# Kernel tuning notes

Hardware: AMD Instinct MI355X
Metric: run time of the kernel (lower is better)

The kernel has to match this reference:

```python
import jax, jax.numpy as jnp
import numpy as np

B, C, NMAX = 256, 1, 256   # graphs, channels, max nodes per graph
N = B * C * NMAX           # total nodes = 65536
E = N * 16                 # edges = 1,048,576
EMB, HID = 128, 128


def setup_inputs() -> dict:
    key = jax.random.key(0)
    ks = jax.random.split(key, 8)
    adj = jax.random.uniform(ks[0], (B, C, NMAX, NMAX), jnp.float32)
    edges = jax.random.randint(ks[1], (E, 2), 0, N, dtype=jnp.int32)
    subgraph_idx = jnp.repeat(jnp.arange(B, dtype=jnp.int32), C * NMAX)
    def lin(k, fan_in, fan_out):
        return jax.random.normal(k, (fan_in, fan_out), jnp.float32) / np.sqrt(fan_in).astype(np.float32)
    return {
        "adj": adj, "edges": edges, "subgraph_idx": subgraph_idx,
        "Wdec": lin(ks[2], NMAX, EMB), "bdec": jnp.zeros((EMB,), jnp.float32),
        "Wc1": lin(ks[3], EMB, HID),   "bc1": jnp.zeros((HID,), jnp.float32),
        "Wc2": lin(ks[4], HID, HID),   "bc2": jnp.zeros((HID,), jnp.float32),
        "Wp1": lin(ks[5], HID, HID),   "bp1": jnp.zeros((HID,), jnp.float32),
        "Wp2": lin(ks[6], HID, 1),     "bp2": jnp.zeros((1,), jnp.float32),
    }


def gcn_conv(x, W, b, src, dst):
    # PyG GCNConv: h = x W; add self-loops; symmetric normalization D^-1/2 (A+I) D^-1/2; + bias
    h = x @ W                                      # [N, out]
    deg = jnp.zeros((N,), x.dtype).at[dst].add(1.0) + 1.0  # in-degree incl. self loop
    dinv = jax.lax.rsqrt(deg)                      # [N]
    coef = dinv[src] * dinv[dst]                   # [E]
    agg = jax.ops.segment_sum(h[src] * coef[:, None], dst, num_segments=N)
    return agg + h * (dinv * dinv)[:, None] + b    # self-loop term + bias


def reference(adj, edges, subgraph_idx, Wdec, bdec, Wc1, bc1, Wc2, bc2, Wp1, bp1, Wp2, bp2):
    src, dst = edges[:, 0], edges[:, 1]
    # decoder_input: Linear(max_num_nodes -> embedding_dim) on flattened adjacency rows
    x = adj.reshape(-1, NMAX) @ Wdec + bdec        # [N, EMB]
    # forward applies convs[:-1] only (2 of the 3 convs); dropout is identity in eval mode
    x = jax.nn.relu(gcn_conv(x, Wc1, bc1, src, dst))
    x = jax.nn.relu(gcn_conv(x, Wc2, bc2, src, dst))
    # global max pool over nodes of each graph
    pooled = jax.ops.segment_max(x, subgraph_idx, num_segments=B)  # [B, HID]
    # post_mp MLP head
    h = jax.nn.relu(pooled @ Wp1 + bp1)
    return h @ Wp2 + bp2                           # [B, 1]
```

## Files before the change

kernel.cpp:

```cpp
#include <hip/hip_runtime.h>
#include <hip/hip_fp16.h>
#include <cstdint>
#include <cstddef>

#define NN   65536
#define NE   1048576
#define FD   128
#define KDEC 256
#define NGRAPH 256
#define NEP_MAX (NE + 15 * NN)
#define DUMMY_SRC 65536u
#define EPB  4096
#define BCAP 4608

typedef __attribute__((ext_vector_type(8))) short s16x8;
typedef __attribute__((ext_vector_type(4))) float f32x4;

__device__ __forceinline__ ushort f2bf(float x) {
  uint u = __float_as_uint(x);
  uint r = (u + 0x7fffu + ((u >> 16) & 1u)) >> 16;
  return (ushort)r;
}
__device__ __forceinline__ float bf2f(ushort h) {
  return __uint_as_float(((uint)h) << 16);
}


__global__ __launch_bounds__(1024) void k_histbin(const int* __restrict__ edges,
                                                  uint* __restrict__ binbuf,
                                                  int* __restrict__ gbin) {
  const int b = blockIdx.x, t = threadIdx.x;
  __shared__ int lcnt[256];
  __shared__ int lsum[256];
  __shared__ int gbase[256];
  __shared__ uint sorted[EPB];

  if (t < 256) lcnt[t] = 0;
  __syncthreads();

  uint rec[4];
  ushort bkt[4], lidx[4];
#pragma unroll
  for (int r = 0; r < 4; r++) {
    int i = b * EPB + r * 1024 + t;
    int2 e = ((const int2*)edges)[i];
    int bucket = e.y >> 8;
    int li = atomicAdd(&lcnt[bucket], 1);
    rec[r] = ((uint)bucket << 24) | ((uint)(e.y & 255) << 16) | (uint)e.x;
    bkt[r] = (ushort)bucket;
    lidx[r] = (ushort)li;
  }
  __syncthreads();

  if (t < 256) lsum[t] = lcnt[t];
  __syncthreads();
  for (int off = 1; off < 256; off <<= 1) {
    int v = 0;
    if (t < 256 && t >= off) v = lsum[t - off];
    __syncthreads();
    if (t < 256) lsum[t] += v;
    __syncthreads();
  }
  if (t < 256) gbase[t] = atomicAdd(&gbin[t], lcnt[t]);
  __syncthreads();

#pragma unroll
  for (int r = 0; r < 4; r++) {
    int B = bkt[r];
    sorted[lsum[B] - lcnt[B] + lidx[r]] = rec[r];
  }
  __syncthreads();

  for (int s = t; s < EPB; s += 1024) {
    uint v = sorted[s];
    int B = v >> 24;
    int ex = lsum[B] - lcnt[B];
    binbuf[B * BCAP + gbase[B] + (s - ex)] = v & 0xFFFFFFu;
  }
}

__device__ __forceinline__ void prep_one(const float* __restrict__ W,
                                         ushort* __restrict__ H,
                                         ushort* __restrict__ L, int i) {
  int k = i >> 7, c = i & 127;
  float w = W[i];
  ushort h = f2bf(w);
  ushort lo = f2bf(w - bf2f(h));
  size_t dst = ((size_t)((k >> 5) * 8 + (c >> 4)) * 64 +
                (size_t)((c & 15) + 16 * ((k & 31) >> 3))) * 8 + (k & 7);
  H[dst] = h;
  L[dst] = lo;
}

__global__ __launch_bounds__(256) void k_misc1(const uint* __restrict__ binbuf,
                                               const int* __restrict__ gbin,
                                               int* __restrict__ hist,
                                               int* __restrict__ bsum,
                                               const float* __restrict__ Wdec,
                                               const float* __restrict__ Wc1,
                                               const float* __restrict__ bdec,
                                               float* __restrict__ wfused,
                                               float* __restrict__ bfused,
                                               const float* __restrict__ Wc2,
                                               ushort* __restrict__ w2h,
                                               ushort* __restrict__ w2l) {
  int b = blockIdx.x, t = threadIdx.x;
  if (b < 256) {
    __shared__ int lc[256];
    __shared__ int s[256];
    lc[t] = 0;
    __syncthreads();
    int m = gbin[b];
    for (int i = t; i < m; i += 256)
      atomicAdd(&lc[binbuf[b * BCAP + i] >> 16], 1);
    __syncthreads();
    hist[b * 256 + t] = lc[t];
    s[t] = (lc[t] + 15) & ~15;
    __syncthreads();
    for (int st = 128; st > 0; st >>= 1) {
      if (t < st) s[t] += s[t + st];
      __syncthreads();
    }
    if (t == 0) bsum[b] = s[0];
  } else if (b < 384) {
    int i = (b - 256) * 256 + t;
    int k = i >> 7, c = i & 127;
    float acc = 0.f;
#pragma unroll 8
    for (int j = 0; j < 128; j++) acc = fmaf(Wdec[k * FD + j], Wc1[j * FD + c], acc);
    wfused[i] = acc;
    if (b == 256 && t < 128) {
      float ba = 0.f;
      for (int j = 0; j < 128; j++) ba = fmaf(bdec[j], Wc1[j * FD + t], ba);
      bfused[t] = ba;
    }
  } else {
    int i = (b - 384) * 256 + t;
    prep_one(Wc2, w2h, w2l, i);
  }
}

__global__ __launch_bounds__(256) void k_misc2(const int* __restrict__ hist,
                                               const int* __restrict__ bsum,
                                               int* __restrict__ offs,
                                               float* __restrict__ dinv,
                                               const float* __restrict__ wfused,
                                               ushort* __restrict__ wfh,
                                               ushort* __restrict__ wfl,
                                               const uint* __restrict__ binbuf,
                                               const int* __restrict__ gbin,
                                               uint* __restrict__ ec) {
  int b = blockIdx.x, t = threadIdx.x;
  if (b < 256) {
    __shared__ int sb[256];
    __shared__ int s[256];
    __shared__ int sofs[256];
    __shared__ int cnt2[256];
    sb[t] = bsum[t];
    int v = hist[b * 256 + t];
    int vp = (v + 15) & ~15;
    s[t] = vp;
    __syncthreads();
    for (int off = 1; off < 256; off <<= 1) {
      int addb = (t >= off) ? sb[t - off] : 0;
      int add = (t >= off) ? s[t - off] : 0;
      __syncthreads();
      sb[t] += addb;
      s[t] += add;
      __syncthreads();
    }
    int pb = (b > 0) ? sb[b - 1] : 0;
    int of = pb + s[t] - vp;
    offs[b * 256 + t] = of;
    sofs[t] = of;
    dinv[b * 256 + t] = rsqrtf((float)(v + 1));
    cnt2[t] = 0;
    __syncthreads();

    int m = gbin[b];
    for (int i = t; i < m; i += 256) {
      uint rec = binbuf[(size_t)b * BCAP + i];
      int dlow = rec >> 16;
      int pos = sofs[dlow] + atomicAdd(&cnt2[dlow], 1);
      ec[pos] = rec & 0xFFFFu;
    }
    __syncthreads();
    int base = sofs[t];
    for (int j = v; j < vp; j++) ec[base + j] = DUMMY_SRC;
  } else {
    int i = (b - 256) * 256 + t;
    prep_one(wfused, wfh, wfl, i);
  }
}


template <bool ASPLIT>
__global__ __launch_bounds__(256) void k_gemm(const void* __restrict__ A0,
                                              const void* __restrict__ A1,
                                              const ushort* __restrict__ Whi,
                                              const ushort* __restrict__ Wlo,
                                              const float* __restrict__ bias,
                                              const float* __restrict__ scale,
                                              ushort* __restrict__ Y, int K) {
  __shared__ ushort Bs[2][8192];
  const int t = threadIdx.x;
  const int w = t >> 6;
  const int l = t & 63;
  const int lr = l & 15;
  const int kg = l >> 4;
  const int r0 = blockIdx.x * 128 + w * 32;
  const int nks = K >> 5;

  f32x4 acc[2][8];
#pragma unroll
  for (int mb = 0; mb < 2; mb++)
#pragma unroll
    for (int nb = 0; nb < 8; nb++) acc[mb][nb] = (f32x4)0.f;

  f32x4 araw[4];
  s16x8 ahn[2], aln[2];
  s16x8 bh0, bh1, bl0, bl1;

  auto issueA = [&](int s) {
#pragma unroll
    for (int mb = 0; mb < 2; mb++) {
      size_t base = (size_t)(r0 + mb * 16 + lr) * K + s * 32 + kg * 8;
      if (ASPLIT) {
        ahn[mb] = *(const s16x8*)((const ushort*)A0 + base);
        aln[mb] = *(const s16x8*)((const ushort*)A1 + base);
      } else {
        const float* xp = (const float*)A0 + base;
        araw[mb * 2] = *(const f32x4*)xp;
        araw[mb * 2 + 1] = *(const f32x4*)(xp + 4);
      }
    }
  };
  auto issueB = [&](int s) {
    const ushort* ph = Whi + (size_t)s * 4096 + t * 16;
    const ushort* pl = Wlo + (size_t)s * 4096 + t * 16;
    bh0 = *(const s16x8*)ph;
    bh1 = *(const s16x8*)(ph + 8);
    bl0 = *(const s16x8*)pl;
    bl1 = *(const s16x8*)(pl + 8);
  };
  auto writeB = [&](int buf) {
    *(s16x8*)&Bs[buf][t * 16] = bh0;
    *(s16x8*)&Bs[buf][t * 16 + 8] = bh1;
    *(s16x8*)&Bs[buf][4096 + t * 16] = bl0;
    *(s16x8*)&Bs[buf][4096 + t * 16 + 8] = bl1;
  };

  issueB(0);
  issueA(0);
  writeB(0);
  __syncthreads();

  int buf = 0;
  for (int s = 0; s < nks; ++s) {
    s16x8 ah[2], al[2];
    if (ASPLIT) {
      ah[0] = ahn[0]; ah[1] = ahn[1];
      al[0] = aln[0]; al[1] = aln[1];
    } else {
#pragma unroll
      for (int mb = 0; mb < 2; mb++) {
        float xv[8] = {araw[mb*2].x, araw[mb*2].y, araw[mb*2].z, araw[mb*2].w,
                       araw[mb*2+1].x, araw[mb*2+1].y, araw[mb*2+1].z, araw[mb*2+1].w};
        union { ushort u[8]; s16x8 v; } H, L;
#pragma unroll
        for (int e = 0; e < 8; e++) {
          ushort h = f2bf(xv[e]);
          H.u[e] = h;
          L.u[e] = f2bf(xv[e] - bf2f(h));
        }
        ah[mb] = H.v;
        al[mb] = L.v;
      }
    }
    const bool more = (s + 1 < nks);
    if (more) { issueB(s + 1); issueA(s + 1); }

#pragma unroll
    for (int nb = 0; nb < 8; nb++) {
      s16x8 bh = *(const s16x8*)&Bs[buf][nb * 512 + l * 8];
      s16x8 bl = *(const s16x8*)&Bs[buf][4096 + nb * 512 + l * 8];
#pragma unroll
      for (int mb = 0; mb < 2; mb++) {
        acc[mb][nb] = __builtin_amdgcn_mfma_f32_16x16x32_bf16(ah[mb], bh, acc[mb][nb], 0, 0, 0);
        acc[mb][nb] = __builtin_amdgcn_mfma_f32_16x16x32_bf16(ah[mb], bl, acc[mb][nb], 0, 0, 0);
        acc[mb][nb] = __builtin_amdgcn_mfma_f32_16x16x32_bf16(al[mb], bh, acc[mb][nb], 0, 0, 0);
      }
    }
    if (more) {
      writeB(buf ^ 1);
      __syncthreads();
      buf ^= 1;
    }
  }

  float dvr[2][4];
#pragma unroll
  for (int mb = 0; mb < 2; mb++)
#pragma unroll
    for (int r = 0; r < 4; r++)
      dvr[mb][r] = scale ? scale[r0 + mb * 16 + kg * 4 + r] : 1.f;

#pragma unroll
  for (int nb = 0; nb < 8; nb++) {
    int col = nb * 16 + lr;
    float bv = bias ? bias[col] : 0.f;
#pragma unroll
    for (int mb = 0; mb < 2; mb++)
#pragma unroll
      for (int r = 0; r < 4; r++) {
        size_t row = (size_t)(r0 + mb * 16 + kg * 4 + r);
        Y[row * FD + col] = f2bf((acc[mb][nb][r] + bv) * dvr[mb][r]);
      }
  }
}


template <int EMIT>
__global__ __launch_bounds__(256) void k_agg(const ushort* __restrict__ h16,
                                             const uint* __restrict__ ec,
                                             const int* __restrict__ offs,
                                             const int* __restrict__ hist,
                                             const float* __restrict__ dinv,
                                             const float* __restrict__ bias,
                                             ushort* __restrict__ yhi,
                                             ushort* __restrict__ ylo,
                                             float* __restrict__ pooled) {
  __shared__ int pmax[128];
  const int t = threadIdx.x;
  if (EMIT == 1) {
    if (t < 128) pmax[t] = 0;
    __syncthreads();
  }
  const int n = blockIdx.x * 4 + (t >> 6);
  const int l = t & 63;
  const int half = l >> 5;
  const int dl = (l & 31) * 4;

  const int cnt_p = (hist[n] + 15) & ~15;
  const uint* ep = ec + offs[n];

  float a0 = 0.f, a1 = 0.f, a2 = 0.f, a3 = 0.f;
  float b0 = 0.f, b1 = 0.f, b2 = 0.f, b3 = 0.f;
  for (int i = half; i < cnt_p; i += 16) {
    uint s0 = ep[i];
    uint s1 = ep[i + 2];
    uint s2 = ep[i + 4];
    uint s3 = ep[i + 6];
    uint s4 = ep[i + 8];
    uint s5 = ep[i + 10];
    uint s6 = ep[i + 12];
    uint s7 = ep[i + 14];
    ushort4 v0 = *(const ushort4*)(h16 + ((size_t)s0 << 7) + dl);
    ushort4 v1 = *(const ushort4*)(h16 + ((size_t)s1 << 7) + dl);
    ushort4 v2 = *(const ushort4*)(h16 + ((size_t)s2 << 7) + dl);
    ushort4 v3 = *(const ushort4*)(h16 + ((size_t)s3 << 7) + dl);
    ushort4 v4 = *(const ushort4*)(h16 + ((size_t)s4 << 7) + dl);
    ushort4 v5 = *(const ushort4*)(h16 + ((size_t)s5 << 7) + dl);
    ushort4 v6 = *(const ushort4*)(h16 + ((size_t)s6 << 7) + dl);
    ushort4 v7 = *(const ushort4*)(h16 + ((size_t)s7 << 7) + dl);
    a0 += bf2f(v0.x); a1 += bf2f(v0.y); a2 += bf2f(v0.z); a3 += bf2f(v0.w);
    b0 += bf2f(v1.x); b1 += bf2f(v1.y); b2 += bf2f(v1.z); b3 += bf2f(v1.w);
    a0 += bf2f(v2.x); a1 += bf2f(v2.y); a2 += bf2f(v2.z); a3 += bf2f(v2.w);
    b0 += bf2f(v3.x); b1 += bf2f(v3.y); b2 += bf2f(v3.z); b3 += bf2f(v3.w);
    a0 += bf2f(v4.x); a1 += bf2f(v4.y); a2 += bf2f(v4.z); a3 += bf2f(v4.w);
    b0 += bf2f(v5.x); b1 += bf2f(v5.y); b2 += bf2f(v5.z); b3 += bf2f(v5.w);
    a0 += bf2f(v6.x); a1 += bf2f(v6.y); a2 += bf2f(v6.z); a3 += bf2f(v6.w);
    b0 += bf2f(v7.x); b1 += bf2f(v7.y); b2 += bf2f(v7.z); b3 += bf2f(v7.w);
  }
  a0 += b0; a1 += b1; a2 += b2; a3 += b3;
  a0 += __shfl_xor(a0, 32);
  a1 += __shfl_xor(a1, 32);
  a2 += __shfl_xor(a2, 32);
  a3 += __shfl_xor(a3, 32);

  if (l < 32) {
    float dv = dinv[n];
    ushort4 vs = *(const ushort4*)(h16 + ((size_t)n << 7) + dl);
    float4 bb = *(const float4*)(bias + dl);
    float o0 = fmaxf(fmaf(dv, a0 + bf2f(vs.x), bb.x), 0.f);
    float o1 = fmaxf(fmaf(dv, a1 + bf2f(vs.y), bb.y), 0.f);
    float o2 = fmaxf(fmaf(dv, a2 + bf2f(vs.z), bb.z), 0.f);
    float o3 = fmaxf(fmaf(dv, a3 + bf2f(vs.w), bb.w), 0.f);
    if (EMIT == 0) {
      ushort4 hi, lo;
      hi.x = f2bf(o0); lo.x = f2bf(o0 - bf2f(hi.x));
      hi.y = f2bf(o1); lo.y = f2bf(o1 - bf2f(hi.y));
      hi.z = f2bf(o2); lo.z = f2bf(o2 - bf2f(hi.z));
      hi.w = f2bf(o3); lo.w = f2bf(o3 - bf2f(hi.w));
      size_t base = (size_t)n * FD + dl;
      *(ushort4*)(yhi + base) = hi;
      *(ushort4*)(ylo + base) = lo;
    } else {
      atomicMax(&pmax[dl + 0], __float_as_int(o0));
      atomicMax(&pmax[dl + 1], __float_as_int(o1));
      atomicMax(&pmax[dl + 2], __float_as_int(o2));
      atomicMax(&pmax[dl + 3], __float_as_int(o3));
    }
  }
  if (EMIT == 1) {
    __syncthreads();
    if (t < 128) {
      int gr = blockIdx.x >> 6;
      atomicMax((int*)pooled + gr * FD + t, pmax[t]);
    }
  }
}


__global__ __launch_bounds__(128) void k_mlp(const float* __restrict__ pooled,
                                             const float* __restrict__ Wp1,
                                             const float* __restrict__ bp1,
                                             const float* __restrict__ Wp2,
                                             const float* __restrict__ bp2,
                                             float* __restrict__ out) {
  __shared__ float row[128];
  __shared__ float red[128];
  int g = blockIdx.x, t = threadIdx.x;
  row[t] = pooled[g * FD + t];
  __syncthreads();
  float acc = bp1[t];
#pragma unroll 8
  for (int k = 0; k < 128; k++) acc = fmaf(row[k], Wp1[k * FD + t], acc);
  acc = fmaxf(acc, 0.f);
  red[t] = acc * Wp2[t];
  __syncthreads();
  for (int st = 64; st > 0; st >>= 1) {
    if (t < st) red[t] += red[t + st];
    __syncthreads();
  }
  if (t == 0) out[g] = red[0] + bp2[0];
}


extern "C" void kernel_launch(void* const* d_in, const int* in_sizes, int n_in,
                              void* d_out, int out_size, void* d_ws, size_t ws_size,
                              hipStream_t stream) {
  (void)in_sizes; (void)n_in; (void)out_size; (void)ws_size;

  const float* adj  = (const float*)d_in[0];
  const int*   edges= (const int*)d_in[1];
  const float* Wdec = (const float*)d_in[3];
  const float* bdec = (const float*)d_in[4];
  const float* Wc1  = (const float*)d_in[5];
  const float* bc1  = (const float*)d_in[6];
  const float* Wc2  = (const float*)d_in[7];
  const float* bc2  = (const float*)d_in[8];
  const float* Wp1  = (const float*)d_in[9];
  const float* bp1  = (const float*)d_in[10];
  const float* Wp2  = (const float*)d_in[11];
  const float* bp2  = (const float*)d_in[12];
  float* out = (float*)d_out;

  char* ws = (char*)d_ws;
  size_t off = 0;
  auto alloc = [&](size_t bytes) -> void* {
    void* p = ws + off;
    off += (bytes + 255) & ~(size_t)255;
    return p;
  };
  ushort* h16  = (ushort*)alloc((size_t)(NN + 1) * FD * 2);
  ushort* x1hi = (ushort*)alloc((size_t)NN * FD * 2);
  ushort* x1lo = (ushort*)alloc((size_t)NN * FD * 2);
  float*  pooled = (float*)alloc((size_t)NGRAPH * FD * 4);
  int*    gbin = (int*)alloc(256 * 4);
  int*    hist = (int*)alloc((size_t)NN * 4);
  int*    offs = (int*)alloc((size_t)NN * 4);
  int*    bsum = (int*)alloc(256 * 4);
  uint*   ec   = (uint*)alloc((size_t)NEP_MAX * 4);
  uint*   binbuf = (uint*)alloc((size_t)256 * BCAP * 4);
  float*  dinv = (float*)alloc((size_t)NN * 4);
  float*  wfused = (float*)alloc((size_t)KDEC * FD * 4);
  float*  bfused = (float*)alloc(FD * 4);
  ushort* wfh = (ushort*)alloc((size_t)KDEC * FD * 2);
  ushort* wfl = (ushort*)alloc((size_t)KDEC * FD * 2);
  ushort* w2h = (ushort*)alloc((size_t)FD * FD * 2);
  ushort* w2l = (ushort*)alloc((size_t)FD * FD * 2);

  hipMemsetAsync(pooled, 0, (size_t)NGRAPH * FD * 4 + 256 * 4, stream);
  hipMemsetAsync(h16 + (size_t)NN * FD, 0, FD * 2, stream);

  k_histbin<<<256, 1024, 0, stream>>>(edges, binbuf, gbin);
  k_misc1<<<448, 256, 0, stream>>>(binbuf, gbin, hist, bsum, Wdec, Wc1, bdec,
                                   wfused, bfused, Wc2, w2h, w2l);
  k_misc2<<<384, 256, 0, stream>>>(hist, bsum, offs, dinv, wfused, wfh, wfl,
                                   binbuf, gbin, ec);

  k_gemm<false><<<NN / 128, 256, 0, stream>>>(adj, nullptr, wfh, wfl, bfused, dinv, h16, KDEC);

  k_agg<0><<<NN / 4, 256, 0, stream>>>(h16, ec, offs, hist, dinv, bc1, x1hi, x1lo, nullptr);

  k_gemm<true><<<NN / 128, 256, 0, stream>>>(x1hi, x1lo, w2h, w2l, nullptr, dinv, h16, FD);

  k_agg<1><<<NN / 4, 256, 0, stream>>>(h16, ec, offs, hist, dinv, bc2, nullptr, nullptr, pooled);

  k_mlp<<<NGRAPH, 128, 0, stream>>>(pooled, Wp1, bp1, Wp2, bp2, out);
}
```

Baseline: 166.5 us.

## Merge CSR-build kernels and fold weight prep into the binning kernel

Moves the weight fusion (Wdec@Wc1) and the bf16 hi/lo splitting of both weight matrices into extra blocks of the edge-binning kernel. The histogram, scan and scatter steps are merged into a single kernel by giving each bucket a fixed padded region of the edge array (BCAPP slots per bucket), which removes the need for a global cross-bucket prefix sum. Two launches and the intermediate wfused and bsum buffers go away. In exchange the padded edge array is larger and sparser, and it relies on each bucket's padded count staying within 8448.

```diff
diff --git a/kernel.cpp b/kernel.cpp
--- a/kernel.cpp
+++ b/kernel.cpp
@@ -8,10 +8,10 @@
 #define FD   128
 #define KDEC 256
 #define NGRAPH 256
-#define NEP_MAX (NE + 15 * NN)
 #define DUMMY_SRC 65536u
 #define EPB  4096
 #define BCAP 4608
+#define BCAPP 8448
 
 typedef __attribute__((ext_vector_type(8))) short s16x8;
 typedef __attribute__((ext_vector_type(4))) float f32x4;
@@ -25,11 +25,49 @@
   return __uint_as_float(((uint)h) << 16);
 }
 
+__device__ __forceinline__ void wsplit(float w, int k, int c,
+                                       ushort* __restrict__ H,
+                                       ushort* __restrict__ L) {
+  ushort h = f2bf(w);
+  size_t dst = ((size_t)((k >> 5) * 8 + (c >> 4)) * 64 +
+                (size_t)((c & 15) + 16 * ((k & 31) >> 3))) * 8 + (k & 7);
+  H[dst] = h;
+  L[dst] = f2bf(w - bf2f(h));
+}
+
 
 __global__ __launch_bounds__(1024) void k_histbin(const int* __restrict__ edges,
                                                   uint* __restrict__ binbuf,
-                                                  int* __restrict__ gbin) {
+                                                  int* __restrict__ gbin,
+                                                  const float* __restrict__ Wdec,
+                                                  const float* __restrict__ Wc1,
+                                                  const float* __restrict__ bdec,
+                                                  float* __restrict__ bfused,
+                                                  ushort* __restrict__ wfh,
+                                                  ushort* __restrict__ wfl,
+                                                  const float* __restrict__ Wc2,
+                                                  ushort* __restrict__ w2h,
+                                                  ushort* __restrict__ w2l) {
   const int b = blockIdx.x, t = threadIdx.x;
+  if (b >= 256) {
+    if (b < 288) {
+      int i = (b - 256) * 1024 + t;
+      int k = i >> 7, c = i & 127;
+      float acc = 0.f;
+#pragma unroll 8
+      for (int j = 0; j < 128; j++) acc = fmaf(Wdec[k * FD + j], Wc1[j * FD + c], acc);
+      wsplit(acc, k, c, wfh, wfl);
+      if (b == 256 && t < 128) {
+        float ba = 0.f;
+        for (int j = 0; j < 128; j++) ba = fmaf(bdec[j], Wc1[j * FD + t], ba);
+        bfused[t] = ba;
+      }
+    } else {
+      int i = (b - 288) * 1024 + t;
+      wsplit(Wc2[i], i >> 7, i & 127, w2h, w2l);
+    }
+    return;
+  }
   __shared__ int lcnt[256];
   __shared__ int lsum[256];
   __shared__ int gbase[256];
@@ -79,118 +117,52 @@
   }
 }
 
-__device__ __forceinline__ void prep_one(const float* __restrict__ W,
-                                         ushort* __restrict__ H,
-                                         ushort* __restrict__ L, int i) {
-  int k = i >> 7, c = i & 127;
-  float w = W[i];
-  ushort h = f2bf(w);
-  ushort lo = f2bf(w - bf2f(h));
-  size_t dst = ((size_t)((k >> 5) * 8 + (c >> 4)) * 64 +
-                (size_t)((c & 15) + 16 * ((k & 31) >> 3))) * 8 + (k & 7);
-  H[dst] = h;
-  L[dst] = lo;
-}
-
-__global__ __launch_bounds__(256) void k_misc1(const uint* __restrict__ binbuf,
-                                               const int* __restrict__ gbin,
-                                               int* __restrict__ hist,
-                                               int* __restrict__ bsum,
-                                               const float* __restrict__ Wdec,
-                                               const float* __restrict__ Wc1,
-                                               const float* __restrict__ bdec,
-                                               float* __restrict__ wfused,
-                                               float* __restrict__ bfused,
-                                               const float* __restrict__ Wc2,
-                                               ushort* __restrict__ w2h,
-                                               ushort* __restrict__ w2l) {
-  int b = blockIdx.x, t = threadIdx.x;
-  if (b < 256) {
-    __shared__ int lc[256];
-    __shared__ int s[256];
-    lc[t] = 0;
-    __syncthreads();
-    int m = gbin[b];
-    for (int i = t; i < m; i += 256)
-      atomicAdd(&lc[binbuf[b * BCAP + i] >> 16], 1);
-    __syncthreads();
-    hist[b * 256 + t] = lc[t];
-    s[t] = (lc[t] + 15) & ~15;
-    __syncthreads();
-    for (int st = 128; st > 0; st >>= 1) {
-      if (t < st) s[t] += s[t + st];
-      __syncthreads();
-    }
-    if (t == 0) bsum[b] = s[0];
-  } else if (b < 384) {
-    int i = (b - 256) * 256 + t;
-    int k = i >> 7, c = i & 127;
-    float acc = 0.f;
-#pragma unroll 8
-    for (int j = 0; j < 128; j++) acc = fmaf(Wdec[k * FD + j], Wc1[j * FD + c], acc);
-    wfused[i] = acc;
-    if (b == 256 && t < 128) {
-      float ba = 0.f;
-      for (int j = 0; j < 128; j++) ba = fmaf(bdec[j], Wc1[j * FD + t], ba);
-      bfused[t] = ba;
-    }
-  } else {
-    int i = (b - 384) * 256 + t;
-    prep_one(Wc2, w2h, w2l, i);
-  }
-}
-
-__global__ __launch_bounds__(256) void k_misc2(const int* __restrict__ hist,
-                                               const int* __restrict__ bsum,
-                                               int* __restrict__ offs,
-                                               float* __restrict__ dinv,
-                                               const float* __restrict__ wfused,
-                                               ushort* __restrict__ wfh,
-                                               ushort* __restrict__ wfl,
-                                               const uint* __restrict__ binbuf,
-                                               const int* __restrict__ gbin,
-                                               uint* __restrict__ ec) {
-  int b = blockIdx.x, t = threadIdx.x;
-  if (b < 256) {
-    __shared__ int sb[256];
-    __shared__ int s[256];
-    __shared__ int sofs[256];
-    __shared__ int cnt2[256];
-    sb[t] = bsum[t];
-    int v = hist[b * 256 + t];
-    int vp = (v + 15) & ~15;
-    s[t] = vp;
-    __syncthreads();
-    for (int off = 1; off < 256; off <<= 1) {
-      int addb = (t >= off) ? sb[t - off] : 0;
-      int add = (t >= off) ? s[t - off] : 0;
-      __syncthreads();
-      sb[t] += addb;
-      s[t] += add;
-      __syncthreads();
-    }
-    int pb = (b > 0) ? sb[b - 1] : 0;
-    int of = pb + s[t] - vp;
-    offs[b * 256 + t] = of;
-    sofs[t] = of;
-    dinv[b * 256 + t] = rsqrtf((float)(v + 1));
-    cnt2[t] = 0;
-    __syncthreads();
-
-    int m = gbin[b];
-    for (int i = t; i < m; i += 256) {
-      uint rec = binbuf[(size_t)b * BCAP + i];
-      int dlow = rec >> 16;
-      int pos = sofs[dlow] + atomicAdd(&cnt2[dlow], 1);
-      ec[pos] = rec & 0xFFFFu;
-    }
-    __syncthreads();
-    int base = sofs[t];
-    for (int j = v; j < vp; j++) ec[base + j] = DUMMY_SRC;
-  } else {
-    int i = (b - 256) * 256 + t;
-    prep_one(wfused, wfh, wfl, i);
-  }
+
+__global__ __launch_bounds__(256) void k_misc(const uint* __restrict__ binbuf,
+                                              const int* __restrict__ gbin,
+                                              int* __restrict__ hist,
+                                              int* __restrict__ offs,
+                                              float* __restrict__ dinv,
+                                              uint* __restrict__ ec) {
+  __shared__ int lc[256];
+  __shared__ int s[256];
+  __shared__ int sofs[256];
+  __shared__ int cnt2[256];
+  const int b = blockIdx.x, t = threadIdx.x;
+  lc[t] = 0;
+  cnt2[t] = 0;
+  __syncthreads();
+  const int m = gbin[b];
+  const uint* bp_ = binbuf + (size_t)b * BCAP;
+  for (int i = t; i < m; i += 256)
+    atomicAdd(&lc[bp_[i] >> 16], 1);
+  __syncthreads();
+  const int v = lc[t];
+  const int vp = (v + 15) & ~15;
+  s[t] = vp;
+  __syncthreads();
+  for (int off = 1; off < 256; off <<= 1) {
+    int add = (t >= off) ? s[t - off] : 0;
+    __syncthreads();
+    s[t] += add;
+    __syncthreads();
+  }
+  const int of = b * BCAPP + s[t] - vp;
+  offs[b * 256 + t] = of;
+  hist[b * 256 + t] = v;
+  dinv[b * 256 + t] = rsqrtf((float)(v + 1));
+  sofs[t] = of;
+  __syncthreads();
+
+  for (int i = t; i < m; i += 256) {
+    uint rec = bp_[i];
+    int dlow = rec >> 16;
+    int pos = sofs[dlow] + atomicAdd(&cnt2[dlow], 1);
+    ec[pos] = rec & 0xFFFFu;
+  }
+  __syncthreads();
+  int base = sofs[t];
+  for (int j = v; j < vp; j++) ec[base + j] = DUMMY_SRC;
 }
 
 
@@ -470,11 +442,9 @@
   int*    gbin = (int*)alloc(256 * 4);
   int*    hist = (int*)alloc((size_t)NN * 4);
   int*    offs = (int*)alloc((size_t)NN * 4);
-  int*    bsum = (int*)alloc(256 * 4);
-  uint*   ec   = (uint*)alloc((size_t)NEP_MAX * 4);
+  uint*   ec   = (uint*)alloc((size_t)256 * BCAPP * 4);
   uint*   binbuf = (uint*)alloc((size_t)256 * BCAP * 4);
   float*  dinv = (float*)alloc((size_t)NN * 4);
-  float*  wfused = (float*)alloc((size_t)KDEC * FD * 4);
   float*  bfused = (float*)alloc(FD * 4);
   ushort* wfh = (ushort*)alloc((size_t)KDEC * FD * 2);
   ushort* wfl = (ushort*)alloc((size_t)KDEC * FD * 2);
@@ -484,11 +454,9 @@
   hipMemsetAsync(pooled, 0, (size_t)NGRAPH * FD * 4 + 256 * 4, stream);
   hipMemsetAsync(h16 + (size_t)NN * FD, 0, FD * 2, stream);
 
-  k_histbin<<<256, 1024, 0, stream>>>(edges, binbuf, gbin);
-  k_misc1<<<448, 256, 0, stream>>>(binbuf, gbin, hist, bsum, Wdec, Wc1, bdec,
-                                   wfused, bfused, Wc2, w2h, w2l);
-  k_misc2<<<384, 256, 0, stream>>>(hist, bsum, offs, dinv, wfused, wfh, wfl,
-                                   binbuf, gbin, ec);
+  k_histbin<<<304, 1024, 0, stream>>>(edges, binbuf, gbin, Wdec, Wc1, bdec,
+                                      bfused, wfh, wfl, Wc2, w2h, w2l);
+  k_misc<<<256, 256, 0, stream>>>(binbuf, gbin, hist, offs, dinv, ec);
 
   k_gemm<false><<<NN / 128, 256, 0, stream>>>(adj, nullptr, wfh, wfl, bfused, dinv, h16, KDEC);
 
```

After: 166.2 us. No clear change (-0.2%).
